# Optimization experiments

Measured on AMD Instinct MI355X. Metric: run time of the kernel, lower is better.

## Reference

```python
import jax, jax.numpy as jnp
import numpy as np

N_NODES = 100000
N_EDGES = 1600000
N_GRAPHS = 256
IN_F = 64   # global_features (GNN input dim)
OUT_F = 64  # node_features (GNN output dim)


def setup_inputs() -> dict:
    key = jax.random.key(0)
    ks = jax.random.split(key, 8)
    x = jax.random.normal(ks[0], (N_NODES, IN_F), dtype=jnp.float32)
    edge_index = jax.random.randint(ks[1], (2, N_EDGES), 0, N_NODES, dtype=jnp.int64)
    batch = jnp.sort(jax.random.randint(ks[2], (N_NODES,), 0, N_GRAPHS, dtype=jnp.int64))
    # GNNLayer linear: in=global_features, out=node_features
    W_gnn = jax.random.normal(ks[3], (IN_F, OUT_F), dtype=jnp.float32) / np.sqrt(IN_F)
    b_gnn = jnp.zeros((OUT_F,), dtype=jnp.float32)
    # global_attention: Linear(node_features, 1)
    W_att = jax.random.normal(ks[4], (OUT_F, 1), dtype=jnp.float32) / np.sqrt(OUT_F)
    b_att = jnp.zeros((1,), dtype=jnp.float32)
    return {"x": x, "edge_index": edge_index, "batch": batch,
            "W_gnn": W_gnn, "b_gnn": b_gnn, "W_att": W_att, "b_att": b_att}


def reference(x, edge_index, batch, W_gnn, b_gnn, W_att, b_att):
    src, dst = edge_index[0], edge_index[1]
    # --- GNN message passing layer: aggregate neighbor features, transform ---
    agg = jax.ops.segment_sum(x[src], dst, num_segments=N_NODES)  # [N, IN_F]
    h = jax.nn.relu((x + agg) @ W_gnn + b_gnn)                    # [N, OUT_F]
    # --- attention scores + scatter softmax over batch segments ---
    scores = (h @ W_att + b_att)[:, 0]                            # [N]
    seg_max = jax.ops.segment_max(scores, batch, num_segments=N_GRAPHS)
    e = jnp.exp(scores - seg_max[batch])
    denom = jax.ops.segment_sum(e, batch, num_segments=N_GRAPHS)
    w = e / denom[batch]                                          # [N]
    # --- weighted scatter-add pooling ---
    out = jax.ops.segment_sum(w[:, None] * h, batch, num_segments=N_GRAPHS)
    return out  # [N_GRAPHS, OUT_F]
```

## Files before the change

kernel.cpp:

```cpp
#include <hip/hip_runtime.h>
#include <hip/hip_cooperative_groups.h>

namespace cg = cooperative_groups;

#define N_NODES  100000
#define N_EDGES  1600000
#define N_GRAPHS 256
#define F        64


#define GRID     1024
#define BLK      256

#define NBUCK    196
#define BCAP     9216
#define BSTRIDE  16

#define EPB      1563
#define REPT     7

#define CAST_ELEMS (N_NODES * F / 4)
#define NODES_PER_WAVE 25

__device__ __forceinline__ unsigned short f2bf(float f) {
    unsigned int u = __float_as_uint(f);
    u += 0x7FFFu + ((u >> 16) & 1u);
    return (unsigned short)(u >> 16);
}
__device__ __forceinline__ float bfl(unsigned int u) { return __uint_as_float(u << 16); }
__device__ __forceinline__ float bfh(unsigned int u) { return __uint_as_float(u & 0xFFFF0000u); }

struct SharedBin {
    int hist[NBUCK]; int roffs[NBUCK]; int bbase[NBUCK]; int curs[NBUCK];
    int wsum[8];
    unsigned int   stage[EPB];
    unsigned short bstage[EPB];
};
struct SharedSort { int hist[512]; int curs[512]; int wsum[8]; };
union SharedU { SharedBin bin; SharedSort sort; };


__device__ __forceinline__ void phase_zero(int bid, int tid,
        float* out, float* denom, int* balloc) {
    int g0 = bid * BLK + tid;
    if (g0 < N_GRAPHS * F) out[g0] = 0.f;
    if (g0 < N_GRAPHS) denom[g0] = 0.f;
    if (g0 < NBUCK) balloc[g0 * BSTRIDE] = 0;
}

__device__ __forceinline__ void phase_bin(int bid, int tid,
        const int* __restrict__ src, const int* __restrict__ dst,
        unsigned int* __restrict__ pairs, int* __restrict__ balloc,
        SharedBin& s) {
    int lane = tid & 63, wv = tid >> 6;
    int base = bid * EPB;
    int m    = min(EPB, N_EDGES - base);

    for (int k = tid; k < NBUCK; k += BLK) s.hist[k] = 0;
    __syncthreads();

    int de[REPT], se[REPT];
    #pragma unroll
    for (int r = 0; r < REPT; ++r) {
        int e = tid + r * BLK;
        if (e < m) {
            de[r] = dst[base + e];
            se[r] = src[base + e];
            atomicAdd(&s.hist[de[r] >> 9], 1);
        } else { de[r] = -1; se[r] = 0; }
    }
    __syncthreads();

    int cnt = (tid < NBUCK) ? s.hist[tid] : 0;
    int v = cnt;
    #pragma unroll
    for (int o = 1; o < 64; o <<= 1) {
        int u = __shfl_up(v, o, 64);
        if (lane >= o) v += u;
    }
    if (lane == 63) s.wsum[wv] = v;
    __syncthreads();
    if (tid < 4) {
        int sv = s.wsum[tid];
        int u = __shfl_up(sv, 1, 64); if (tid >= 1) sv += u;
        u     = __shfl_up(sv, 2, 64); if (tid >= 2) sv += u;
        s.wsum[tid] = sv;
    }
    __syncthreads();
    if (wv > 0) v += s.wsum[wv - 1];
    if (tid < NBUCK) {
        int excl = v - cnt;
        s.roffs[tid] = excl;
        s.curs[tid]  = excl;
        s.bbase[tid] = tid * BCAP + atomicAdd(&balloc[tid * BSTRIDE], cnt);
    }
    __syncthreads();

    #pragma unroll
    for (int r = 0; r < REPT; ++r) {
        if (de[r] >= 0) {
            int bk  = de[r] >> 9;
            int pos = atomicAdd(&s.curs[bk], 1);
            s.stage[pos]  = ((unsigned)(de[r] & 511) << 17) | (unsigned)se[r];
            s.bstage[pos] = (unsigned short)bk;
        }
    }
    __syncthreads();
    for (int e = tid; e < m; e += BLK) {
        int bk = s.bstage[e];
        pairs[s.bbase[bk] + (e - s.roffs[bk])] = s.stage[e];
    }
}

__device__ __forceinline__ void phase_sortcast(int bid, int tid,
        const float* __restrict__ x, unsigned short* __restrict__ xh,
        const unsigned int* __restrict__ pairs, int* __restrict__ eidx,
        int* __restrict__ nbeg, int* __restrict__ nend,
        const int* __restrict__ balloc, SharedSort& s) {
    int lane = tid & 63, wv = tid >> 6;
    if (bid < NBUCK) {
        int E     = balloc[bid * BSTRIDE];
        int base  = bid * BCAP;
        int node0 = bid << 9;
        int nn    = min(512, N_NODES - node0);

        s.hist[tid] = 0; s.hist[tid + 256] = 0;
        __syncthreads();
        for (int i = tid; i < E; i += BLK)
            atomicAdd(&s.hist[pairs[base + i] >> 17], 1);
        __syncthreads();

        int c0 = s.hist[tid];
        int v0 = c0;
        #pragma unroll
        for (int o = 1; o < 64; o <<= 1) { int u = __shfl_up(v0, o, 64); if (lane >= o) v0 += u; }
        if (lane == 63) s.wsum[wv] = v0;
        __syncthreads();
        if (tid < 4) {
            int sv = s.wsum[tid];
            int u = __shfl_up(sv, 1, 64); if (tid >= 1) sv += u;
            u     = __shfl_up(sv, 2, 64); if (tid >= 2) sv += u;
            s.wsum[tid] = sv;
        }
        __syncthreads();
        if (wv > 0) v0 += s.wsum[wv - 1];
        int total0 = s.wsum[3];

        int c1 = s.hist[tid + 256];
        int v1 = c1;
        #pragma unroll
        for (int o = 1; o < 64; o <<= 1) { int u = __shfl_up(v1, o, 64); if (lane >= o) v1 += u; }
        if (lane == 63) s.wsum[4 + wv] = v1;
        __syncthreads();
        if (tid < 4) {
            int sv = s.wsum[4 + tid];
            int u = __shfl_up(sv, 1, 64); if (tid >= 1) sv += u;
            u     = __shfl_up(sv, 2, 64); if (tid >= 2) sv += u;
            s.wsum[4 + tid] = sv;
        }
        __syncthreads();
        if (wv > 0) v1 += s.wsum[4 + wv - 1];
        v1 += total0;

        int e0 = v0 - c0, e1 = v1 - c1;
        s.curs[tid] = e0; s.curs[tid + 256] = e1;
        if (tid < nn)       { nbeg[node0 + tid] = base + e0;
                              nend[node0 + tid] = base + e0 + c0; }
        if (tid + 256 < nn) { nbeg[node0 + tid + 256] = base + e1;
                              nend[node0 + tid + 256] = base + e1 + c1; }
        __syncthreads();

        for (int i = tid; i < E; i += BLK) {
            unsigned int p = pairs[base + i];
            int pos = atomicAdd(&s.curs[p >> 17], 1);
            eidx[base + pos] = (int)(p & 0x1FFFFu);
        }
    } else {
        int i0      = (bid - NBUCK) * BLK + tid;
        int cstride = (GRID - NBUCK) * BLK;
        for (int i = i0; i < CAST_ELEMS; i += cstride) {
            float4 v4 = ((const float4*)x)[i];
            ushort4 o;
            o.x = f2bf(v4.x); o.y = f2bf(v4.y); o.z = f2bf(v4.z); o.w = f2bf(v4.w);
            ((ushort4*)xh)[i] = o;
        }
    }
}

__device__ __forceinline__ void phase_gather(int bid, int tid,
        const unsigned short* __restrict__ xh,
        const int* __restrict__ nbeg, const int* __restrict__ nend,
        const int* __restrict__ eidx, const int* __restrict__ batch,
        const float* __restrict__ Wg, const float* __restrict__ bg,
        const float* __restrict__ Wa, const float* __restrict__ ba,
        float* __restrict__ out, float* __restrict__ denom) {
    int lane = tid & 63;
    int grp  = lane >> 3;
    int c    = lane & 7;
    int waveId = bid * 4 + (tid >> 6);
    int n0 = waveId * NODES_PER_WAVE;
    if (n0 >= N_NODES) return;
    int nEnd = min(n0 + NODES_PER_WAVE, N_NODES);

    float wcol[F];
    #pragma unroll
    for (int k = 0; k < F; ++k) wcol[k] = Wg[k * F + lane];
    float bgl = bg[lane];
    float wal = Wa[lane];
    float ba0 = ba[0];

    const uint4* xh4 = (const uint4*)xh;

    int   cur_g = batch[n0];
    float accw  = 0.f;
    float denw  = 0.f;

    int pb = nbeg[n0];
    int pe = nend[n0];
    int sl_cur = (pb + lane < pe) ? eidx[pb + lane] : 0;

    for (int n = n0; n < nEnd; ++n) {
        int start = pb, end = pe;
        int sl    = sl_cur;
        if (n + 1 < nEnd) {
            pb = nbeg[n + 1];
            pe = nend[n + 1];
            sl_cur = (pb + lane < pe) ? eidx[pb + lane] : 0;
        }

        float a0=0.f,a1=0.f,a2=0.f,a3=0.f,a4=0.f,a5=0.f,a6=0.f,a7=0.f;
        {
            int jmax = end - start; if (jmax > 64) jmax = 64;
            for (int j = 0; j < jmax; j += 8) {
                int el = j + grp;
                int sidx = __shfl(sl, el, 64);
                if (el < jmax) {
                    uint4 v = xh4[sidx * 8 + c];
                    a0 += bfl(v.x); a1 += bfh(v.x);
                    a2 += bfl(v.y); a3 += bfh(v.y);
                    a4 += bfl(v.z); a5 += bfh(v.z);
                    a6 += bfl(v.w); a7 += bfh(v.w);
                }
            }
        }
        for (int base2 = start + 64; base2 < end; base2 += 64) {
            int jmax = end - base2; if (jmax > 64) jmax = 64;
            int sl2 = (base2 + lane < end) ? eidx[base2 + lane] : 0;
            for (int j = 0; j < jmax; j += 8) {
                int el = j + grp;
                int sidx = __shfl(sl2, el, 64);
                if (el < jmax) {
                    uint4 v = xh4[sidx * 8 + c];
                    a0 += bfl(v.x); a1 += bfh(v.x);
                    a2 += bfl(v.y); a3 += bfh(v.y);
                    a4 += bfl(v.z); a5 += bfh(v.z);
                    a6 += bfl(v.w); a7 += bfh(v.w);
                }
            }
        }
        #pragma unroll
        for (int o = 8; o <= 32; o <<= 1) {
            a0 += __shfl_xor(a0, o, 64); a1 += __shfl_xor(a1, o, 64);
            a2 += __shfl_xor(a2, o, 64); a3 += __shfl_xor(a3, o, 64);
            a4 += __shfl_xor(a4, o, 64); a5 += __shfl_xor(a5, o, 64);
            a6 += __shfl_xor(a6, o, 64); a7 += __shfl_xor(a7, o, 64);
        }
        {
            uint4 v = xh4[n * 8 + c];
            a0 += bfl(v.x); a1 += bfh(v.x);
            a2 += bfl(v.y); a3 += bfh(v.y);
            a4 += bfl(v.z); a5 += bfh(v.z);
            a6 += bfl(v.w); a7 += bfh(v.w);
        }

        float re[8] = {a0,a1,a2,a3,a4,a5,a6,a7};
        float q0=0.f,q1=0.f,q2=0.f,q3=0.f,q4=0.f,q5=0.f,q6=0.f,q7=0.f;
        #pragma unroll
        for (int k = 0; k < F; k += 8) {
            int ln = k >> 3;
            q0 += __int_as_float(__builtin_amdgcn_readlane(__float_as_int(re[0]), ln)) * wcol[k + 0];
            q1 += __int_as_float(__builtin_amdgcn_readlane(__float_as_int(re[1]), ln)) * wcol[k + 1];
            q2 += __int_as_float(__builtin_amdgcn_readlane(__float_as_int(re[2]), ln)) * wcol[k + 2];
            q3 += __int_as_float(__builtin_amdgcn_readlane(__float_as_int(re[3]), ln)) * wcol[k + 3];
            q4 += __int_as_float(__builtin_amdgcn_readlane(__float_as_int(re[4]), ln)) * wcol[k + 4];
            q5 += __int_as_float(__builtin_amdgcn_readlane(__float_as_int(re[5]), ln)) * wcol[k + 5];
            q6 += __int_as_float(__builtin_amdgcn_readlane(__float_as_int(re[6]), ln)) * wcol[k + 6];
            q7 += __int_as_float(__builtin_amdgcn_readlane(__float_as_int(re[7]), ln)) * wcol[k + 7];
        }
        float hv = ((q0 + q1) + (q2 + q3)) + ((q4 + q5) + (q6 + q7)) + bgl;
        hv = hv > 0.f ? hv : 0.f;

        float p = hv * wal;
        #pragma unroll
        for (int o = 32; o > 0; o >>= 1)
            p += __shfl_down(p, o, 64);
        float sc = __int_as_float(__builtin_amdgcn_readlane(__float_as_int(p), 0)) + ba0;
        float e = __expf(sc);

        int g = batch[n];
        if (g != cur_g) {
            atomicAdd(&out[cur_g * F + lane], accw);
            if (lane == 0) atomicAdd(&denom[cur_g], denw);
            accw = 0.f; denw = 0.f; cur_g = g;
        }
        accw += e * hv;
        denw += e;
    }
    atomicAdd(&out[cur_g * F + lane], accw);
    if (lane == 0) atomicAdd(&denom[cur_g], denw);
}

__device__ __forceinline__ void phase_fin(int bid, int tid,
        float* out, const float* denom) {
    int g0 = bid * BLK + tid;
    if (g0 < N_GRAPHS * F) {
        float d = denom[g0 >> 6];
        out[g0] = (d > 0.f) ? out[g0] / d : 0.f;
    }
}

__global__ __launch_bounds__(BLK, 4) void fused_kernel(
        const float* __restrict__ x,
        const int* __restrict__ src, const int* __restrict__ dst,
        const int* __restrict__ batch,
        const float* __restrict__ Wg, const float* __restrict__ bg,
        const float* __restrict__ Wa, const float* __restrict__ ba,
        float* __restrict__ out,
        unsigned short* __restrict__ xh,
        unsigned int* __restrict__ pairs, int* __restrict__ eidx,
        int* __restrict__ nbeg, int* __restrict__ nend,
        int* __restrict__ balloc, float* __restrict__ denom) {
    cg::grid_group grid = cg::this_grid();
    __shared__ SharedU sh;
    int tid = threadIdx.x, bid = blockIdx.x;

    phase_zero(bid, tid, out, denom, balloc);
    __threadfence(); grid.sync(); __threadfence();

    phase_bin(bid, tid, src, dst, pairs, balloc, sh.bin);
    __threadfence(); grid.sync(); __threadfence();

    phase_sortcast(bid, tid, x, xh, pairs, eidx, nbeg, nend, balloc, sh.sort);
    __threadfence(); grid.sync(); __threadfence();

    phase_gather(bid, tid, xh, nbeg, nend, eidx, batch, Wg, bg, Wa, ba, out, denom);
    __threadfence(); grid.sync(); __threadfence();

    phase_fin(bid, tid, out, denom);
}

__global__ __launch_bounds__(BLK) void k_zero(float* out, float* denom, int* balloc) {
    phase_zero(blockIdx.x, threadIdx.x, out, denom, balloc);
}
__global__ __launch_bounds__(BLK) void k_bin(const int* src, const int* dst,
        unsigned int* pairs, int* balloc) {
    __shared__ SharedBin s;
    phase_bin(blockIdx.x, threadIdx.x, src, dst, pairs, balloc, s);
}
__global__ __launch_bounds__(BLK) void k_sortcast(const float* x, unsigned short* xh,
        const unsigned int* pairs, int* eidx, int* nbeg, int* nend, const int* balloc) {
    __shared__ SharedSort s;
    phase_sortcast(blockIdx.x, threadIdx.x, x, xh, pairs, eidx, nbeg, nend, balloc, s);
}
__global__ __launch_bounds__(BLK) void k_gather(const unsigned short* xh,
        const int* nbeg, const int* nend, const int* eidx, const int* batch,
        const float* Wg, const float* bg, const float* Wa, const float* ba,
        float* out, float* denom) {
    phase_gather(blockIdx.x, threadIdx.x, xh, nbeg, nend, eidx, batch,
                 Wg, bg, Wa, ba, out, denom);
}
__global__ __launch_bounds__(BLK) void k_fin(float* out, const float* denom) {
    phase_fin(blockIdx.x, threadIdx.x, out, denom);
}

extern "C" void kernel_launch(void* const* d_in, const int* in_sizes, int n_in,
                              void* d_out, int out_size, void* d_ws, size_t ws_size,
                              hipStream_t stream) {
    const float* x     = (const float*)d_in[0];
    const int*   ei    = (const int*)d_in[1];
    const int*   batch = (const int*)d_in[2];
    const float* Wg    = (const float*)d_in[3];
    const float* bg    = (const float*)d_in[4];
    const float* Wa    = (const float*)d_in[5];
    const float* ba    = (const float*)d_in[6];
    float* out = (float*)d_out;

    const int* src = ei;
    const int* dst = ei + N_EDGES;

    char* ws = (char*)d_ws;
    unsigned short* xh     = (unsigned short*)(ws);
    unsigned int*   pairs  = (unsigned int*)(ws + 12800000);
    int*            eidx   = (int*)(ws + 20025344);
    int*            nbeg   = (int*)(ws + 27250688);
    int*            nend   = (int*)(ws + 27652096);
    int*            balloc = (int*)(ws + 28053504);
    float*          denom  = (float*)(ws + 28066048);

    static int s_path = -1;
    if (s_path < 0) {
        int dev = 0; hipGetDevice(&dev);
        int coop = 0;
        hipDeviceGetAttribute(&coop, hipDeviceAttributeCooperativeLaunch, dev);
        int ncu = 0;
        hipDeviceGetAttribute(&ncu, hipDeviceAttributeMultiprocessorCount, dev);
        int maxB = 0;
        hipOccupancyMaxActiveBlocksPerMultiprocessor(&maxB, fused_kernel, BLK, 0);
        s_path = (coop != 0 && (long)maxB * (long)ncu >= GRID) ? 1 : 0;
    }

    if (s_path == 1) {
        void* kargs[] = {
            (void*)&x, (void*)&src, (void*)&dst, (void*)&batch,
            (void*)&Wg, (void*)&bg, (void*)&Wa, (void*)&ba,
            (void*)&out, (void*)&xh, (void*)&pairs, (void*)&eidx,
            (void*)&nbeg, (void*)&nend, (void*)&balloc, (void*)&denom
        };
        hipError_t err = hipLaunchCooperativeKernel(fused_kernel, dim3(GRID),
                                                    dim3(BLK), kargs, 0, stream);
        if (err != hipSuccess) s_path = 0;
    }
    if (s_path == 0) {
        k_zero    <<<64,   BLK, 0, stream>>>(out, denom, balloc);
        k_bin     <<<GRID, BLK, 0, stream>>>(src, dst, pairs, balloc);
        k_sortcast<<<GRID, BLK, 0, stream>>>(x, xh, pairs, eidx, nbeg, nend, balloc);
        k_gather  <<<GRID, BLK, 0, stream>>>(xh, nbeg, nend, eidx, batch,
                                             Wg, bg, Wa, ba, out, denom);
        k_fin     <<<64,   BLK, 0, stream>>>(out, denom);
    }
}
```

Before: 213.1 us.

## Replace cooperative fused kernel with separate launches and MFMA-based node transform

Drops the cooperative grid-synced fused kernel in favour of a memset plus four ordinary kernel launches, and folds the output and denominator zeroing into the sortcast kernel. The gather stage now has each wave aggregate 16 nodes at a time with per-lane 2-byte loads, stores the aggregate as split hi/lo bf16 in LDS, and computes the 64x64 linear layer with bf16 MFMA instructions instead of per-lane FMA loops with readlane broadcasts. Pooling atomics are issued once per graph per 16-node tile rather than per wave run. The hi/lo split keeps precision near fp32 at the cost of twice the MFMA work, and the narrower 2-byte gather loads may raise the number of memory transactions.

```diff
diff --git a/kernel.cpp b/kernel.cpp
--- a/kernel.cpp
+++ b/kernel.cpp
@@ -1,7 +1,4 @@
 #include <hip/hip_runtime.h>
-#include <hip/hip_cooperative_groups.h>
-
-namespace cg = cooperative_groups;
 
 #define N_NODES  100000
 #define N_EDGES  1600000
@@ -9,54 +6,43 @@
 #define F        64
 
 
-#define GRID     1024
+#define GRID_PRE 1024
 #define BLK      256
 
 #define NBUCK    196
 #define BCAP     9216
 #define BSTRIDE  16
-
 #define EPB      1563
 #define REPT     7
 
 #define CAST_ELEMS (N_NODES * F / 4)
-#define NODES_PER_WAVE 25
+#define NT_BLOCKS  ((N_NODES + 63) / 64)
+
+typedef short  bf16x8 __attribute__((ext_vector_type(8)));
+typedef float  f32x4  __attribute__((ext_vector_type(4)));
 
 __device__ __forceinline__ unsigned short f2bf(float f) {
     unsigned int u = __float_as_uint(f);
     u += 0x7FFFu + ((u >> 16) & 1u);
     return (unsigned short)(u >> 16);
 }
-__device__ __forceinline__ float bfl(unsigned int u) { return __uint_as_float(u << 16); }
-__device__ __forceinline__ float bfh(unsigned int u) { return __uint_as_float(u & 0xFFFF0000u); }
-
-struct SharedBin {
-    int hist[NBUCK]; int roffs[NBUCK]; int bbase[NBUCK]; int curs[NBUCK];
-    int wsum[8];
-    unsigned int   stage[EPB];
-    unsigned short bstage[EPB];
-};
-struct SharedSort { int hist[512]; int curs[512]; int wsum[8]; };
-union SharedU { SharedBin bin; SharedSort sort; };
-
-
-__device__ __forceinline__ void phase_zero(int bid, int tid,
-        float* out, float* denom, int* balloc) {
-    int g0 = bid * BLK + tid;
-    if (g0 < N_GRAPHS * F) out[g0] = 0.f;
-    if (g0 < N_GRAPHS) denom[g0] = 0.f;
-    if (g0 < NBUCK) balloc[g0 * BSTRIDE] = 0;
-}
-
-__device__ __forceinline__ void phase_bin(int bid, int tid,
+__device__ __forceinline__ float bfu(unsigned short u) {
+    return __uint_as_float((unsigned)u << 16);
+}
+
+__global__ __launch_bounds__(BLK) void bin_kernel(
         const int* __restrict__ src, const int* __restrict__ dst,
-        unsigned int* __restrict__ pairs, int* __restrict__ balloc,
-        SharedBin& s) {
+        unsigned int* __restrict__ pairs, int* __restrict__ balloc) {
+    __shared__ int hist[NBUCK], roffs[NBUCK], bbase[NBUCK], curs[NBUCK];
+    __shared__ int wsum[8];
+    __shared__ unsigned int   stage[EPB];
+    __shared__ unsigned short bstage[EPB];
+    int tid = threadIdx.x, bid = blockIdx.x;
     int lane = tid & 63, wv = tid >> 6;
     int base = bid * EPB;
-    int m    = min(EPB, N_EDGES - base);
-
-    for (int k = tid; k < NBUCK; k += BLK) s.hist[k] = 0;
+    int m = min(EPB, N_EDGES - base);
+
+    for (int k = tid; k < NBUCK; k += BLK) hist[k] = 0;
     __syncthreads();
 
     int de[REPT], se[REPT];
@@ -66,33 +52,30 @@
         if (e < m) {
             de[r] = dst[base + e];
             se[r] = src[base + e];
-            atomicAdd(&s.hist[de[r] >> 9], 1);
+            atomicAdd(&hist[de[r] >> 9], 1);
         } else { de[r] = -1; se[r] = 0; }
     }
     __syncthreads();
 
-    int cnt = (tid < NBUCK) ? s.hist[tid] : 0;
+    int cnt = (tid < NBUCK) ? hist[tid] : 0;
     int v = cnt;
     #pragma unroll
-    for (int o = 1; o < 64; o <<= 1) {
-        int u = __shfl_up(v, o, 64);
-        if (lane >= o) v += u;
-    }
-    if (lane == 63) s.wsum[wv] = v;
+    for (int o = 1; o < 64; o <<= 1) { int u = __shfl_up(v, o, 64); if (lane >= o) v += u; }
+    if (lane == 63) wsum[wv] = v;
     __syncthreads();
     if (tid < 4) {
-        int sv = s.wsum[tid];
+        int sv = wsum[tid];
         int u = __shfl_up(sv, 1, 64); if (tid >= 1) sv += u;
         u     = __shfl_up(sv, 2, 64); if (tid >= 2) sv += u;
-        s.wsum[tid] = sv;
-    }
-    __syncthreads();
-    if (wv > 0) v += s.wsum[wv - 1];
+        wsum[tid] = sv;
+    }
+    __syncthreads();
+    if (wv > 0) v += wsum[wv - 1];
     if (tid < NBUCK) {
         int excl = v - cnt;
-        s.roffs[tid] = excl;
-        s.curs[tid]  = excl;
-        s.bbase[tid] = tid * BCAP + atomicAdd(&balloc[tid * BSTRIDE], cnt);
+        roffs[tid] = excl;
+        curs[tid]  = excl;
+        bbase[tid] = tid * BCAP + atomicAdd(&balloc[tid * BSTRIDE], cnt);
     }
     __syncthreads();
 
@@ -100,70 +83,74 @@
     for (int r = 0; r < REPT; ++r) {
         if (de[r] >= 0) {
             int bk  = de[r] >> 9;
-            int pos = atomicAdd(&s.curs[bk], 1);
-            s.stage[pos]  = ((unsigned)(de[r] & 511) << 17) | (unsigned)se[r];
-            s.bstage[pos] = (unsigned short)bk;
+            int pos = atomicAdd(&curs[bk], 1);
+            stage[pos]  = ((unsigned)(de[r] & 511) << 17) | (unsigned)se[r];
+            bstage[pos] = (unsigned short)bk;
         }
     }
     __syncthreads();
     for (int e = tid; e < m; e += BLK) {
-        int bk = s.bstage[e];
-        pairs[s.bbase[bk] + (e - s.roffs[bk])] = s.stage[e];
-    }
-}
-
-__device__ __forceinline__ void phase_sortcast(int bid, int tid,
+        int bk = bstage[e];
+        pairs[bbase[bk] + (e - roffs[bk])] = stage[e];
+    }
+}
+
+__global__ __launch_bounds__(BLK) void sortcast_kernel(
         const float* __restrict__ x, unsigned short* __restrict__ xh,
         const unsigned int* __restrict__ pairs, int* __restrict__ eidx,
         int* __restrict__ nbeg, int* __restrict__ nend,
-        const int* __restrict__ balloc, SharedSort& s) {
+        const int* __restrict__ balloc,
+        float* __restrict__ out, float* __restrict__ denom) {
+    __shared__ int hist[512], curs[512], wsum[8];
+    int tid = threadIdx.x, bid = blockIdx.x;
     int lane = tid & 63, wv = tid >> 6;
+
     if (bid < NBUCK) {
         int E     = balloc[bid * BSTRIDE];
         int base  = bid * BCAP;
         int node0 = bid << 9;
         int nn    = min(512, N_NODES - node0);
 
-        s.hist[tid] = 0; s.hist[tid + 256] = 0;
+        hist[tid] = 0; hist[tid + 256] = 0;
         __syncthreads();
         for (int i = tid; i < E; i += BLK)
-            atomicAdd(&s.hist[pairs[base + i] >> 17], 1);
-        __syncthreads();
-
-        int c0 = s.hist[tid];
+            atomicAdd(&hist[pairs[base + i] >> 17], 1);
+        __syncthreads();
+
+        int c0 = hist[tid];
         int v0 = c0;
         #pragma unroll
         for (int o = 1; o < 64; o <<= 1) { int u = __shfl_up(v0, o, 64); if (lane >= o) v0 += u; }
-        if (lane == 63) s.wsum[wv] = v0;
+        if (lane == 63) wsum[wv] = v0;
         __syncthreads();
         if (tid < 4) {
-            int sv = s.wsum[tid];
+            int sv = wsum[tid];
             int u = __shfl_up(sv, 1, 64); if (tid >= 1) sv += u;
             u     = __shfl_up(sv, 2, 64); if (tid >= 2) sv += u;
-            s.wsum[tid] = sv;
-        }
-        __syncthreads();
-        if (wv > 0) v0 += s.wsum[wv - 1];
-        int total0 = s.wsum[3];
-
-        int c1 = s.hist[tid + 256];
+            wsum[tid] = sv;
+        }
+        __syncthreads();
+        if (wv > 0) v0 += wsum[wv - 1];
+        int total0 = wsum[3];
+
+        int c1 = hist[tid + 256];
         int v1 = c1;
         #pragma unroll
         for (int o = 1; o < 64; o <<= 1) { int u = __shfl_up(v1, o, 64); if (lane >= o) v1 += u; }
-        if (lane == 63) s.wsum[4 + wv] = v1;
+        if (lane == 63) wsum[4 + wv] = v1;
         __syncthreads();
         if (tid < 4) {
-            int sv = s.wsum[4 + tid];
+            int sv = wsum[4 + tid];
             int u = __shfl_up(sv, 1, 64); if (tid >= 1) sv += u;
             u     = __shfl_up(sv, 2, 64); if (tid >= 2) sv += u;
-            s.wsum[4 + tid] = sv;
-        }
-        __syncthreads();
-        if (wv > 0) v1 += s.wsum[4 + wv - 1];
+            wsum[4 + tid] = sv;
+        }
+        __syncthreads();
+        if (wv > 0) v1 += wsum[4 + wv - 1];
         v1 += total0;
 
         int e0 = v0 - c0, e1 = v1 - c1;
-        s.curs[tid] = e0; s.curs[tid + 256] = e1;
+        curs[tid] = e0; curs[tid + 256] = e1;
         if (tid < nn)       { nbeg[node0 + tid] = base + e0;
                               nend[node0 + tid] = base + e0 + c0; }
         if (tid + 256 < nn) { nbeg[node0 + tid + 256] = base + e1;
@@ -172,12 +159,16 @@
 
         for (int i = tid; i < E; i += BLK) {
             unsigned int p = pairs[base + i];
-            int pos = atomicAdd(&s.curs[p >> 17], 1);
+            int pos = atomicAdd(&curs[p >> 17], 1);
             eidx[base + pos] = (int)(p & 0x1FFFFu);
         }
     } else {
+        if (bid == NBUCK) {
+            for (int i = tid; i < N_GRAPHS * F; i += BLK) out[i] = 0.f;
+            denom[tid] = 0.f;
+        }
         int i0      = (bid - NBUCK) * BLK + tid;
-        int cstride = (GRID - NBUCK) * BLK;
+        int cstride = (GRID_PRE - NBUCK) * BLK;
         for (int i = i0; i < CAST_ELEMS; i += cstride) {
             float4 v4 = ((const float4*)x)[i];
             ushort4 o;
@@ -187,190 +178,200 @@
     }
 }
 
-__device__ __forceinline__ void phase_gather(int bid, int tid,
+__global__ __launch_bounds__(BLK) void gather_mfma_kernel(
         const unsigned short* __restrict__ xh,
-        const int* __restrict__ nbeg, const int* __restrict__ nend,
-        const int* __restrict__ eidx, const int* __restrict__ batch,
-        const float* __restrict__ Wg, const float* __restrict__ bg,
-        const float* __restrict__ Wa, const float* __restrict__ ba,
-        float* __restrict__ out, float* __restrict__ denom) {
+        const int*   __restrict__ nbeg,
+        const int*   __restrict__ nend,
+        const int*   __restrict__ eidx,
+        const int*   __restrict__ batch,
+        const float* __restrict__ Wg,
+        const float* __restrict__ bg,
+        const float* __restrict__ Wa,
+        const float* __restrict__ ba,
+        float*       __restrict__ out,
+        float*       __restrict__ denom) {
+    __shared__ unsigned short shAhi[64 * 64];
+    __shared__ unsigned short shAlo[64 * 64];
+    __shared__ unsigned short shW[64 * 64];
+
+    int tid  = threadIdx.x;
+    int bid  = blockIdx.x;
     int lane = tid & 63;
-    int grp  = lane >> 3;
-    int c    = lane & 7;
-    int waveId = bid * 4 + (tid >> 6);
-    int n0 = waveId * NODES_PER_WAVE;
-    if (n0 >= N_NODES) return;
-    int nEnd = min(n0 + NODES_PER_WAVE, N_NODES);
-
-    float wcol[F];
-    #pragma unroll
-    for (int k = 0; k < F; ++k) wcol[k] = Wg[k * F + lane];
-    float bgl = bg[lane];
-    float wal = Wa[lane];
-    float ba0 = ba[0];
-
-    const uint4* xh4 = (const uint4*)xh;
-
-    int   cur_g = batch[n0];
-    float accw  = 0.f;
-    float denw  = 0.f;
-
-    int pb = nbeg[n0];
-    int pe = nend[n0];
-    int sl_cur = (pb + lane < pe) ? eidx[pb + lane] : 0;
-
-    for (int n = n0; n < nEnd; ++n) {
-        int start = pb, end = pe;
-        int sl    = sl_cur;
-        if (n + 1 < nEnd) {
-            pb = nbeg[n + 1];
-            pe = nend[n + 1];
-            sl_cur = (pb + lane < pe) ? eidx[pb + lane] : 0;
-        }
-
-        float a0=0.f,a1=0.f,a2=0.f,a3=0.f,a4=0.f,a5=0.f,a6=0.f,a7=0.f;
-        {
-            int jmax = end - start; if (jmax > 64) jmax = 64;
-            for (int j = 0; j < jmax; j += 8) {
-                int el = j + grp;
-                int sidx = __shfl(sl, el, 64);
-                if (el < jmax) {
-                    uint4 v = xh4[sidx * 8 + c];
-                    a0 += bfl(v.x); a1 += bfh(v.x);
-                    a2 += bfl(v.y); a3 += bfh(v.y);
-                    a4 += bfl(v.z); a5 += bfh(v.z);
-                    a6 += bfl(v.w); a7 += bfh(v.w);
+    int w    = tid >> 6;
+
+    for (int i = tid; i < 64 * 64; i += BLK) {
+        int k = i >> 6, n = i & 63;
+        shW[n * 64 + k] = f2bf(Wg[i]);
+    }
+    __syncthreads();
+
+    int tile_base = bid * 64 + w * 16;
+    if (tile_base >= N_NODES) return;
+
+    int nb = 0, ne = 0;
+    {
+        int nd = tile_base + lane;
+        if (lane < 16 && nd < N_NODES) { nb = nbeg[nd]; ne = nend[nd]; }
+    }
+    int pb_c = __builtin_amdgcn_readlane(nb, 0);
+    int pe_c = __builtin_amdgcn_readlane(ne, 0);
+    int sl_c = (pb_c + lane < pe_c) ? eidx[pb_c + lane] : 0;
+
+    for (int q = 0; q < 16; ++q) {
+        int node = tile_base + q;
+        int pb = pb_c, pe = pe_c, sl = sl_c;
+        if (q + 1 < 16) {
+            pb_c = __builtin_amdgcn_readlane(nb, q + 1);
+            pe_c = __builtin_amdgcn_readlane(ne, q + 1);
+            sl_c = (pb_c + lane < pe_c) ? eidx[pb_c + lane] : 0;
+        }
+        float y = 0.f;
+        if (node < N_NODES) {
+            y = bfu(xh[node * 64 + lane]);
+            int c0 = min(pe - pb, 64);
+            int e = 0;
+            for (; e + 8 <= c0; e += 8) {
+                int i0 = __builtin_amdgcn_readlane(sl, e + 0);
+                int i1 = __builtin_amdgcn_readlane(sl, e + 1);
+                int i2 = __builtin_amdgcn_readlane(sl, e + 2);
+                int i3 = __builtin_amdgcn_readlane(sl, e + 3);
+                int i4 = __builtin_amdgcn_readlane(sl, e + 4);
+                int i5 = __builtin_amdgcn_readlane(sl, e + 5);
+                int i6 = __builtin_amdgcn_readlane(sl, e + 6);
+                int i7 = __builtin_amdgcn_readlane(sl, e + 7);
+                float v0 = bfu(xh[i0 * 64 + lane]);
+                float v1 = bfu(xh[i1 * 64 + lane]);
+                float v2 = bfu(xh[i2 * 64 + lane]);
+                float v3 = bfu(xh[i3 * 64 + lane]);
+                float v4 = bfu(xh[i4 * 64 + lane]);
+                float v5 = bfu(xh[i5 * 64 + lane]);
+                float v6 = bfu(xh[i6 * 64 + lane]);
+                float v7 = bfu(xh[i7 * 64 + lane]);
+                y += ((v0 + v1) + (v2 + v3)) + ((v4 + v5) + (v6 + v7));
+            }
+            for (; e < c0; ++e) {
+                int i0 = __builtin_amdgcn_readlane(sl, e);
+                y += bfu(xh[i0 * 64 + lane]);
+            }
+            for (int b2 = pb + 64; b2 < pe; b2 += 64) {
+                int sl2 = (b2 + lane < pe) ? eidx[b2 + lane] : 0;
+                int c2 = min(pe - b2, 64);
+                int e2 = 0;
+                for (; e2 + 8 <= c2; e2 += 8) {
+                    int i0 = __builtin_amdgcn_readlane(sl2, e2 + 0);
+                    int i1 = __builtin_amdgcn_readlane(sl2, e2 + 1);
+                    int i2 = __builtin_amdgcn_readlane(sl2, e2 + 2);
+                    int i3 = __builtin_amdgcn_readlane(sl2, e2 + 3);
+                    int i4 = __builtin_amdgcn_readlane(sl2, e2 + 4);
+                    int i5 = __builtin_amdgcn_readlane(sl2, e2 + 5);
+                    int i6 = __builtin_amdgcn_readlane(sl2, e2 + 6);
+                    int i7 = __builtin_amdgcn_readlane(sl2, e2 + 7);
+                    float v0 = bfu(xh[i0 * 64 + lane]);
+                    float v1 = bfu(xh[i1 * 64 + lane]);
+                    float v2 = bfu(xh[i2 * 64 + lane]);
+                    float v3 = bfu(xh[i3 * 64 + lane]);
+                    float v4 = bfu(xh[i4 * 64 + lane]);
+                    float v5 = bfu(xh[i5 * 64 + lane]);
+                    float v6 = bfu(xh[i6 * 64 + lane]);
+                    float v7 = bfu(xh[i7 * 64 + lane]);
+                    y += ((v0 + v1) + (v2 + v3)) + ((v4 + v5) + (v6 + v7));
+                }
+                for (; e2 < c2; ++e2) {
+                    int i0 = __builtin_amdgcn_readlane(sl2, e2);
+                    y += bfu(xh[i0 * 64 + lane]);
                 }
             }
         }
-        for (int base2 = start + 64; base2 < end; base2 += 64) {
-            int jmax = end - base2; if (jmax > 64) jmax = 64;
-            int sl2 = (base2 + lane < end) ? eidx[base2 + lane] : 0;
-            for (int j = 0; j < jmax; j += 8) {
-                int el = j + grp;
-                int sidx = __shfl(sl2, el, 64);
-                if (el < jmax) {
-                    uint4 v = xh4[sidx * 8 + c];
-                    a0 += bfl(v.x); a1 += bfh(v.x);
-                    a2 += bfl(v.y); a3 += bfh(v.y);
-                    a4 += bfl(v.z); a5 += bfh(v.z);
-                    a6 += bfl(v.w); a7 += bfh(v.w);
-                }
-            }
-        }
+        unsigned short hh = f2bf(y);
+        float lo = y - bfu(hh);
+        unsigned short hl = f2bf(lo);
+        shAhi[(w * 16 + q) * 64 + lane] = hh;
+        shAlo[(w * 16 + q) * 64 + lane] = hl;
+    }
+
+    int lr = lane & 15, lq = lane >> 4;
+    const bf16x8 ah0 = *(const bf16x8*)&shAhi[(w * 16 + lr) * 64 +  0 + 8 * lq];
+    const bf16x8 ah1 = *(const bf16x8*)&shAhi[(w * 16 + lr) * 64 + 32 + 8 * lq];
+    const bf16x8 al0 = *(const bf16x8*)&shAlo[(w * 16 + lr) * 64 +  0 + 8 * lq];
+    const bf16x8 al1 = *(const bf16x8*)&shAlo[(w * 16 + lr) * 64 + 32 + 8 * lq];
+
+    f32x4 acc0 = {0.f,0.f,0.f,0.f}, acc1 = {0.f,0.f,0.f,0.f};
+    f32x4 acc2 = {0.f,0.f,0.f,0.f}, acc3 = {0.f,0.f,0.f,0.f};
+    #define DO_TILE(t, accv) { \
+        bf16x8 b0 = *(const bf16x8*)&shW[(16*(t) + lr) * 64 +  0 + 8 * lq]; \
+        bf16x8 b1 = *(const bf16x8*)&shW[(16*(t) + lr) * 64 + 32 + 8 * lq]; \
+        accv = __builtin_amdgcn_mfma_f32_16x16x32_bf16(ah0, b0, accv, 0, 0, 0); \
+        accv = __builtin_amdgcn_mfma_f32_16x16x32_bf16(al0, b0, accv, 0, 0, 0); \
+        accv = __builtin_amdgcn_mfma_f32_16x16x32_bf16(ah1, b1, accv, 0, 0, 0); \
+        accv = __builtin_amdgcn_mfma_f32_16x16x32_bf16(al1, b1, accv, 0, 0, 0); }
+    DO_TILE(0, acc0) DO_TILE(1, acc1) DO_TILE(2, acc2) DO_TILE(3, acc3)
+    #undef DO_TILE
+
+    float bg0 = bg[lr], bg1 = bg[16 + lr], bg2 = bg[32 + lr], bg3 = bg[48 + lr];
+    float wa0 = Wa[lr], wa1 = Wa[16 + lr], wa2 = Wa[32 + lr], wa3 = Wa[48 + lr];
+    float ba0 = ba[0];
+
+    float hv0[4], hv1[4], hv2[4], hv3[4];
+    #pragma unroll
+    for (int r = 0; r < 4; ++r) {
+        hv0[r] = fmaxf(acc0[r] + bg0, 0.f);
+        hv1[r] = fmaxf(acc1[r] + bg1, 0.f);
+        hv2[r] = fmaxf(acc2[r] + bg2, 0.f);
+        hv3[r] = fmaxf(acc3[r] + bg3, 0.f);
+    }
+    float part[4];
+    #pragma unroll
+    for (int r = 0; r < 4; ++r)
+        part[r] = hv0[r] * wa0 + hv1[r] * wa1 + hv2[r] * wa2 + hv3[r] * wa3;
+    #pragma unroll
+    for (int o = 1; o <= 8; o <<= 1) {
         #pragma unroll
-        for (int o = 8; o <= 32; o <<= 1) {
-            a0 += __shfl_xor(a0, o, 64); a1 += __shfl_xor(a1, o, 64);
-            a2 += __shfl_xor(a2, o, 64); a3 += __shfl_xor(a3, o, 64);
-            a4 += __shfl_xor(a4, o, 64); a5 += __shfl_xor(a5, o, 64);
-            a6 += __shfl_xor(a6, o, 64); a7 += __shfl_xor(a7, o, 64);
-        }
-        {
-            uint4 v = xh4[n * 8 + c];
-            a0 += bfl(v.x); a1 += bfh(v.x);
-            a2 += bfl(v.y); a3 += bfh(v.y);
-            a4 += bfl(v.z); a5 += bfh(v.z);
-            a6 += bfl(v.w); a7 += bfh(v.w);
-        }
-
-        float re[8] = {a0,a1,a2,a3,a4,a5,a6,a7};
-        float q0=0.f,q1=0.f,q2=0.f,q3=0.f,q4=0.f,q5=0.f,q6=0.f,q7=0.f;
+        for (int r = 0; r < 4; ++r) part[r] += __shfl_xor(part[r], o, 64);
+    }
+    float ev[4]; int gidx[4];
+    #pragma unroll
+    for (int r = 0; r < 4; ++r) {
+        int node = tile_base + 4 * lq + r;
+        bool ok = node < N_NODES;
+        ev[r]   = ok ? __expf(part[r] + ba0) : 0.f;
+        gidx[r] = ok ? batch[node] : 0;
+    }
+    int gmin = batch[tile_base];
+    int glast = tile_base + 15; if (glast >= N_NODES) glast = N_NODES - 1;
+    int gmax = batch[glast];
+
+    for (int gg = gmin; gg <= gmax; ++gg) {
+        float w0 = (gidx[0] == gg) ? ev[0] : 0.f;
+        float w1 = (gidx[1] == gg) ? ev[1] : 0.f;
+        float w2 = (gidx[2] == gg) ? ev[2] : 0.f;
+        float w3 = (gidx[3] == gg) ? ev[3] : 0.f;
+        float p0 = w0 * hv0[0] + w1 * hv0[1] + w2 * hv0[2] + w3 * hv0[3];
+        float p1 = w0 * hv1[0] + w1 * hv1[1] + w2 * hv1[2] + w3 * hv1[3];
+        float p2 = w0 * hv2[0] + w1 * hv2[1] + w2 * hv2[2] + w3 * hv2[3];
+        float p3 = w0 * hv3[0] + w1 * hv3[1] + w2 * hv3[2] + w3 * hv3[3];
+        float dn = w0 + w1 + w2 + w3;
         #pragma unroll
-        for (int k = 0; k < F; k += 8) {
-            int ln = k >> 3;
-            q0 += __int_as_float(__builtin_amdgcn_readlane(__float_as_int(re[0]), ln)) * wcol[k + 0];
-            q1 += __int_as_float(__builtin_amdgcn_readlane(__float_as_int(re[1]), ln)) * wcol[k + 1];
-            q2 += __int_as_float(__builtin_amdgcn_readlane(__float_as_int(re[2]), ln)) * wcol[k + 2];
-            q3 += __int_as_float(__builtin_amdgcn_readlane(__float_as_int(re[3]), ln)) * wcol[k + 3];
-            q4 += __int_as_float(__builtin_amdgcn_readlane(__float_as_int(re[4]), ln)) * wcol[k + 4];
-            q5 += __int_as_float(__builtin_amdgcn_readlane(__float_as_int(re[5]), ln)) * wcol[k + 5];
-            q6 += __int_as_float(__builtin_amdgcn_readlane(__float_as_int(re[6]), ln)) * wcol[k + 6];
-            q7 += __int_as_float(__builtin_amdgcn_readlane(__float_as_int(re[7]), ln)) * wcol[k + 7];
-        }
-        float hv = ((q0 + q1) + (q2 + q3)) + ((q4 + q5) + (q6 + q7)) + bgl;
-        hv = hv > 0.f ? hv : 0.f;
-
-        float p = hv * wal;
-        #pragma unroll
-        for (int o = 32; o > 0; o >>= 1)
-            p += __shfl_down(p, o, 64);
-        float sc = __int_as_float(__builtin_amdgcn_readlane(__float_as_int(p), 0)) + ba0;
-        float e = __expf(sc);
-
-        int g = batch[n];
-        if (g != cur_g) {
-            atomicAdd(&out[cur_g * F + lane], accw);
-            if (lane == 0) atomicAdd(&denom[cur_g], denw);
-            accw = 0.f; denw = 0.f; cur_g = g;
-        }
-        accw += e * hv;
-        denw += e;
-    }
-    atomicAdd(&out[cur_g * F + lane], accw);
-    if (lane == 0) atomicAdd(&denom[cur_g], denw);
-}
-
-__device__ __forceinline__ void phase_fin(int bid, int tid,
-        float* out, const float* denom) {
-    int g0 = bid * BLK + tid;
-    if (g0 < N_GRAPHS * F) {
-        float d = denom[g0 >> 6];
-        out[g0] = (d > 0.f) ? out[g0] / d : 0.f;
-    }
-}
-
-__global__ __launch_bounds__(BLK, 4) void fused_kernel(
-        const float* __restrict__ x,
-        const int* __restrict__ src, const int* __restrict__ dst,
-        const int* __restrict__ batch,
-        const float* __restrict__ Wg, const float* __restrict__ bg,
-        const float* __restrict__ Wa, const float* __restrict__ ba,
-        float* __restrict__ out,
-        unsigned short* __restrict__ xh,
-        unsigned int* __restrict__ pairs, int* __restrict__ eidx,
-        int* __restrict__ nbeg, int* __restrict__ nend,
-        int* __restrict__ balloc, float* __restrict__ denom) {
-    cg::grid_group grid = cg::this_grid();
-    __shared__ SharedU sh;
-    int tid = threadIdx.x, bid = blockIdx.x;
-
-    phase_zero(bid, tid, out, denom, balloc);
-    __threadfence(); grid.sync(); __threadfence();
-
-    phase_bin(bid, tid, src, dst, pairs, balloc, sh.bin);
-    __threadfence(); grid.sync(); __threadfence();
-
-    phase_sortcast(bid, tid, x, xh, pairs, eidx, nbeg, nend, balloc, sh.sort);
-    __threadfence(); grid.sync(); __threadfence();
-
-    phase_gather(bid, tid, xh, nbeg, nend, eidx, batch, Wg, bg, Wa, ba, out, denom);
-    __threadfence(); grid.sync(); __threadfence();
-
-    phase_fin(bid, tid, out, denom);
-}
-
-__global__ __launch_bounds__(BLK) void k_zero(float* out, float* denom, int* balloc) {
-    phase_zero(blockIdx.x, threadIdx.x, out, denom, balloc);
-}
-__global__ __launch_bounds__(BLK) void k_bin(const int* src, const int* dst,
-        unsigned int* pairs, int* balloc) {
-    __shared__ SharedBin s;
-    phase_bin(blockIdx.x, threadIdx.x, src, dst, pairs, balloc, s);
-}
-__global__ __launch_bounds__(BLK) void k_sortcast(const float* x, unsigned short* xh,
-        const unsigned int* pairs, int* eidx, int* nbeg, int* nend, const int* balloc) {
-    __shared__ SharedSort s;
-    phase_sortcast(blockIdx.x, threadIdx.x, x, xh, pairs, eidx, nbeg, nend, balloc, s);
-}
-__global__ __launch_bounds__(BLK) void k_gather(const unsigned short* xh,
-        const int* nbeg, const int* nend, const int* eidx, const int* batch,
-        const float* Wg, const float* bg, const float* Wa, const float* ba,
-        float* out, float* denom) {
-    phase_gather(blockIdx.x, threadIdx.x, xh, nbeg, nend, eidx, batch,
-                 Wg, bg, Wa, ba, out, denom);
-}
-__global__ __launch_bounds__(BLK) void k_fin(float* out, const float* denom) {
-    phase_fin(blockIdx.x, threadIdx.x, out, denom);
+        for (int o = 16; o <= 32; o <<= 1) {
+            p0 += __shfl_xor(p0, o, 64); p1 += __shfl_xor(p1, o, 64);
+            p2 += __shfl_xor(p2, o, 64); p3 += __shfl_xor(p3, o, 64);
+            dn += __shfl_xor(dn, o, 64);
+        }
+        if (lq == 0) {
+            atomicAdd(&out[gg * F +  0 + lr], p0);
+            atomicAdd(&out[gg * F + 16 + lr], p1);
+            atomicAdd(&out[gg * F + 32 + lr], p2);
+            atomicAdd(&out[gg * F + 48 + lr], p3);
+            if (lr == 0) atomicAdd(&denom[gg], dn);
+        }
+    }
+}
+
+__global__ __launch_bounds__(BLK) void fin_kernel(
+        float* __restrict__ out, const float* __restrict__ denom) {
+    int i = blockIdx.x * BLK + threadIdx.x;
+    if (i >= N_GRAPHS * F) return;
+    float d = denom[i >> 6];
+    out[i] = (d > 0.f) ? out[i] / d : 0.f;
 }
 
 extern "C" void kernel_launch(void* const* d_in, const int* in_sizes, int n_in,
@@ -397,35 +398,11 @@
     int*            balloc = (int*)(ws + 28053504);
     float*          denom  = (float*)(ws + 28066048);
 
-    static int s_path = -1;
-    if (s_path < 0) {
-        int dev = 0; hipGetDevice(&dev);
-        int coop = 0;
-        hipDeviceGetAttribute(&coop, hipDeviceAttributeCooperativeLaunch, dev);
-        int ncu = 0;
-        hipDeviceGetAttribute(&ncu, hipDeviceAttributeMultiprocessorCount, dev);
-        int maxB = 0;
-        hipOccupancyMaxActiveBlocksPerMultiprocessor(&maxB, fused_kernel, BLK, 0);
-        s_path = (coop != 0 && (long)maxB * (long)ncu >= GRID) ? 1 : 0;
-    }
-
-    if (s_path == 1) {
-        void* kargs[] = {
-            (void*)&x, (void*)&src, (void*)&dst, (void*)&batch,
-            (void*)&Wg, (void*)&bg, (void*)&Wa, (void*)&ba,
-            (void*)&out, (void*)&xh, (void*)&pairs, (void*)&eidx,
-            (void*)&nbeg, (void*)&nend, (void*)&balloc, (void*)&denom
-        };
-        hipError_t err = hipLaunchCooperativeKernel(fused_kernel, dim3(GRID),
-                                                    dim3(BLK), kargs, 0, stream);
-        if (err != hipSuccess) s_path = 0;
-    }
-    if (s_path == 0) {
-        k_zero    <<<64,   BLK, 0, stream>>>(out, denom, balloc);
-        k_bin     <<<GRID, BLK, 0, stream>>>(src, dst, pairs, balloc);
-        k_sortcast<<<GRID, BLK, 0, stream>>>(x, xh, pairs, eidx, nbeg, nend, balloc);
-        k_gather  <<<GRID, BLK, 0, stream>>>(xh, nbeg, nend, eidx, batch,
-                                             Wg, bg, Wa, ba, out, denom);
-        k_fin     <<<64,   BLK, 0, stream>>>(out, denom);
-    }
-}
+    hipMemsetAsync(balloc, 0, NBUCK * BSTRIDE * sizeof(int), stream);
+    bin_kernel      <<<GRID_PRE, BLK, 0, stream>>>(src, dst, pairs, balloc);
+    sortcast_kernel <<<GRID_PRE, BLK, 0, stream>>>(x, xh, pairs, eidx,
+                                                   nbeg, nend, balloc, out, denom);
+    gather_mfma_kernel<<<NT_BLOCKS, BLK, 0, stream>>>(xh, nbeg, nend, eidx, batch,
+                                                      Wg, bg, Wa, ba, out, denom);
+    fin_kernel      <<<64, BLK, 0, stream>>>(out, denom);
+}
```

Measured after the change: 222.0 us. 1.04x slower.
